# Kernel tuning notes

Hardware: AMD Instinct MI355X
Metric: run time of the kernel (lower is better)

## Reference

```python
import jax, jax.numpy as jnp
import numpy as np

BLOCK_SIZE = 32
FORMAT_MAX = 1.0
MANTISSA_BITS = 3.0   # E4M3-like element quantization
CYCLE_BUDGET = 16.0   # B_final: MSD cycle budget per output channel
ONLINE_DELAY = 2.0    # delta: online multiplier startup delay
NEG_LOG2 = -60.0


def _safe_log2(x):
    # log2 mapping 0 / negative to a large negative number
    return jnp.where(x > 0, jnp.log2(jnp.maximum(x, 1e-45)), NEG_LOG2)


def _quantize_elements(xn):
    # round-to-nearest float with MANTISSA_BITS mantissa bits (values in [-1, 1])
    a = jnp.abs(xn)
    e = jnp.floor(_safe_log2(a))
    step = jnp.exp2(e - MANTISSA_BITS)
    return jnp.where(a > 0, jnp.round(xn / step) * step, 0.0)


def _quantize_to_blocks(x_blocks, eps=1e-30):
    # x_blocks: (..., nb, bs) -> (x_q same shape, scales (..., nb))
    max_abs = jnp.max(jnp.abs(x_blocks), axis=-1)
    scales = jnp.maximum(max_abs / FORMAT_MAX, eps)
    x_q = _quantize_elements(x_blocks / scales[..., None])
    return x_q, scales


def _compute_inter_block_delays(w_scales, x_scales):
    # w_scales: (out, nb), x_scales: (N, nb)
    combined_log2 = _safe_log2(x_scales)[:, None, :] + _safe_log2(w_scales)[None, :, :]
    combined_e = jnp.floor(combined_log2)                 # (N, out, nb)
    e_max = jnp.max(combined_e, axis=-1)                  # (N, out)
    return e_max[..., None] - combined_e, e_max


def _compute_intra_block_delays(x_q_blocks):
    # x_q_blocks: (N, nb, bs)
    abs_vals = jnp.abs(x_q_blocks)
    elem_log2 = jnp.where(abs_vals > 0,
                          jnp.floor(jnp.log2(jnp.maximum(abs_vals, 1e-45))),
                          NEG_LOG2)
    e_max_block = jnp.max(elem_log2, axis=-1, keepdims=True)
    return e_max_block - elem_log2


def _msd_truncate(value, num_digits):
    # keep the `num_digits` most-significant NAF (non-adjacent form) digits
    abs_v = jnp.abs(value)
    sign = jnp.sign(value)
    mask = (num_digits > 0) & (abs_v > 0)
    msb_pos = jnp.floor(jnp.log2(jnp.maximum(abs_v, 1e-45)))
    scale_up = jnp.exp2(jnp.clip(23.0 - msb_pos, -126.0, 126.0))
    x_scaled = jnp.round(abs_v * scale_up).astype(jnp.int32)   # ~2^23..2^24
    x_h = x_scaled >> 1
    s = x_scaled + x_h
    naf_pos = s & ~x_h
    naf_neg = x_h & ~s
    combined = naf_pos | naf_neg
    naf_width = jnp.where(
        combined > 0,
        jnp.floor(jnp.log2(jnp.maximum(combined.astype(jnp.float32), 1.0))).astype(jnp.int32) + 1,
        jnp.zeros_like(combined))
    drop = jnp.clip(naf_width - num_digits.astype(jnp.int32), 0, 31)
    keep_mask = ~((jnp.int32(1) << drop) - 1)
    recon = ((naf_pos & keep_mask).astype(jnp.float32)
             - (naf_neg & keep_mask).astype(jnp.float32)) / scale_up
    return jnp.where(mask, sign * recon, 0.0)


def setup_inputs() -> dict:
    key = jax.random.key(0)
    k1, k2, k3 = jax.random.split(key, 3)
    N, in_f, out_f = 128, 1024, 512
    x = jax.random.normal(k1, (N, in_f), dtype=jnp.float32)
    weight = jax.random.normal(k2, (out_f, in_f), dtype=jnp.float32) * 0.02
    bias = jax.random.normal(k3, (out_f,), dtype=jnp.float32) * 0.01
    return {"x": x, "weight": weight, "bias": bias}


def reference(x, weight, bias):
    N, in_f = x.shape
    out_f = weight.shape[0]
    nb = in_f // BLOCK_SIZE
    xb = x.reshape(N, nb, BLOCK_SIZE)
    wb = weight.reshape(out_f, nb, BLOCK_SIZE)
    x_q, x_s = _quantize_to_blocks(xb)   # (N, nb, bs), (N, nb)
    w_q, w_s = _quantize_to_blocks(wb)   # (out, nb, bs), (out, nb)
    inter, e_max = _compute_inter_block_delays(w_s, x_s)  # (N, out, nb)
    intra = _compute_intra_block_delays(x_q)              # (N, nb, bs)
    # effective NAF digit budget per product element
    eff = (CYCLE_BUDGET - ONLINE_DELAY) - inter[..., None] - intra[:, None, :, :]
    prod = x_q[:, None, :, :] * w_q[None, :, :, :]        # (N, out, nb, bs)
    trunc = jax.lax.stop_gradient(_msd_truncate(prod, eff))  # torch.no_grad
    block_dots = jnp.sum(trunc, axis=-1)                  # (N, out, nb)
    out = jnp.einsum('nb,ob,nob->no', x_s, w_s, block_dots) + bias
    return out
```

## Files before the change

kernel.cpp:

```cpp
#include <hip/hip_runtime.h>
#include <cstdint>


#define NN 128
#define KF 1024
#define OF 512
#define NB 32
#define KS 32


__global__ __launch_bounds__(256) void prep_kernel(
    const float* __restrict__ x, const float* __restrict__ w,
    uint2* __restrict__ xaP2, uint2* __restrict__ wB,
    float* __restrict__ lxT, float* __restrict__ lw) {
  int bid = blockIdx.x;
  int tid = (int)threadIdx.x;
  bool is_x = bid < 512;
  int eid = is_x ? bid * 256 + tid : (bid - 512) * 256 + tid;
  float v = is_x ? x[eid] : w[eid];
  float a = fabsf(v);
  float m = a;
  #pragma unroll
  for (int s = 1; s < 32; s <<= 1) m = fmaxf(m, __shfl_xor(m, s, 32));
  float scale = fmaxf(m, 1e-30f);
  float xn = v / scale;
  unsigned nb_ = __float_as_uint(xn);
  unsigned ab = nb_ & 0x7fffffffu;
  bool zz = ab < 0x00800000u;
  int e = (int)(ab >> 23) - 127;
  float am = __uint_as_float((ab & 0x007fffffu) | 0x3f800000u);
  int mi = (int)rintf(am * 8.0f);
  if (mi == 16) { mi = 8; ++e; }
  if (zz) mi = 0;
  unsigned sgn = nb_ & 0x80000000u;
  unsigned sb = __float_as_uint(scale);
  if (is_x) {
    int di = zz ? 63 : min(-e, 63);
    unsigned fb = zz ? 0u : ((sb + (((unsigned)e) << 23)) | sgn);
    unsigned meta = (unsigned)mi | ((unsigned)di << 8);
    int k = eid & 1023, n = eid >> 10;
    xaP2[((k >> 1) * NN + n) * 2 + (k & 1)] = make_uint2(fb, meta);
    if ((tid & 31) == 0) lxT[(k >> 5) * NN + n] = log2f(scale);
  } else {
    unsigned fb = zz ? 0u : ((sb + (((unsigned)(e - 7)) << 23)) | sgn);
    wB[eid] = make_uint2(fb, (unsigned)mi);
    int o = eid >> 10, k = eid & 1023;
    if ((tid & 31) == 0) lw[o * NB + (k >> 5)] = log2f(scale);
  }
}

__global__ __launch_bounds__(256) void emax_kernel(
    const float* __restrict__ lxT, const float* __restrict__ lw,
    float* __restrict__ emaxT) {
  int gid = blockIdx.x * 256 + (int)threadIdx.x;
  int n = gid & (NN - 1), o = gid >> 7;
  float m = -1e30f;
  #pragma unroll
  for (int b = 0; b < NB; ++b)
    m = fmaxf(m, floorf(lxT[b * NN + n] + lw[o * NB + b]));
  emaxT[o * NN + n] = m;
}

__device__ __forceinline__ void prod_acc(int mx, int di, float fxs,
                                         unsigned fwbits, int mw, int nb,
                                         float& acc) {
  int p  = __mul24(mx, mw);
  int s3 = (p << 1) + p;
  int cx = s3 ^ p;
  int wd = 32 - __clz(cx);
  int u  = wd + di + nb;
  int drop = min(max(u, 0), wd);
  unsigned keep = 0xFFFFFFFFu << drop;
  unsigned kc = keep & (unsigned)cx;
  int r = (int)((unsigned)s3 & kc) - (int)((unsigned)p & kc);
  acc = fmaf((float)r * fxs, __uint_as_float(fwbits), acc);
}

__global__ __launch_bounds__(256, 4) void main_kernel(
    const uint4* __restrict__ xaP, const uint2* __restrict__ wB,
    const float* __restrict__ lxT, const float* __restrict__ lw,
    const float* __restrict__ emaxT, float* __restrict__ part) {
  __shared__ __align__(16) uint2 tile[32 * 32];
  int bid = blockIdx.x;
  int s   = bid & 31;
  int og  = (bid >> 5) & 15;
  int ng  = bid >> 9;
  int tid = (int)threadIdx.x, lane = tid & 63, w4 = tid >> 6;
  int o_base = og * 32;
  int k0 = s * 32;
  int n = ng * 64 + lane;

  {
    int r = tid >> 3, c = tid & 7;
    const uint4* src = reinterpret_cast<const uint4*>(&wB[(o_base + r) * KF + k0]);
    uint4* dst = reinterpret_cast<uint4*>(&tile[r * 32]);
    dst[c] = src[c];
    dst[c + 8] = src[c + 8];
  }

  int ow = o_base + w4 * 8;
  float lxv = lxT[s * NN + n];
  float acc[8];
  int nbv[8];
  #pragma unroll
  for (int j = 0; j < 8; ++j) {
    acc[j] = 0.f;
    float em = emaxT[(ow + j) * NN + n];
    nbv[j] = -(int)(14.0f - em + floorf(lxv + lw[(ow + j) * NB + s]));
  }
  __syncthreads();

  const uint4* xaRow = &xaP[(size_t)(k0 >> 1) * NN + n];
#define LDT(j, g) (*reinterpret_cast<const uint4*>(&tile[(w4 * 8 + (j)) * 32 + 2 * (g)]))
#define COMPUTE4(xv, t0, t1, t2, t3, J)                                    \
  {                                                                        \
    int mx0 = (int)(xv.y & 255u), di0 = (int)(xv.y >> 8);                  \
    int mx1 = (int)(xv.w & 255u), di1 = (int)(xv.w >> 8);                  \
    float fx0 = __uint_as_float(xv.x), fx1 = __uint_as_float(xv.z);        \
    prod_acc(mx0, di0, fx0, t0.x, (int)t0.y, nbv[J + 0], acc[J + 0]);      \
    prod_acc(mx1, di1, fx1, t0.z, (int)t0.w, nbv[J + 0], acc[J + 0]);      \
    prod_acc(mx0, di0, fx0, t1.x, (int)t1.y, nbv[J + 1], acc[J + 1]);      \
    prod_acc(mx1, di1, fx1, t1.z, (int)t1.w, nbv[J + 1], acc[J + 1]);      \
    prod_acc(mx0, di0, fx0, t2.x, (int)t2.y, nbv[J + 2], acc[J + 2]);      \
    prod_acc(mx1, di1, fx1, t2.z, (int)t2.w, nbv[J + 2], acc[J + 2]);      \
    prod_acc(mx0, di0, fx0, t3.x, (int)t3.y, nbv[J + 3], acc[J + 3]);      \
    prod_acc(mx1, di1, fx1, t3.z, (int)t3.w, nbv[J + 3], acc[J + 3]);      \
  }

  uint4 xa_ = xaRow[0];
  #pragma unroll 1
  for (int g = 0; g < 16; ++g) {
    uint4 xn_ = xaRow[(size_t)(g + 1) * NN];
    {
      uint4 t0 = LDT(0, g), t1 = LDT(1, g), t2 = LDT(2, g), t3 = LDT(3, g);
      COMPUTE4(xa_, t0, t1, t2, t3, 0);
    }
    {
      uint4 t0 = LDT(4, g), t1 = LDT(5, g), t2 = LDT(6, g), t3 = LDT(7, g);
      COMPUTE4(xa_, t0, t1, t2, t3, 4);
    }
    xa_ = xn_;
  }

  #pragma unroll
  for (int j = 0; j < 8; ++j)
    part[((size_t)(s * OF) + ow + j) * NN + n] = acc[j];
#undef COMPUTE4
#undef LDT
}

__global__ __launch_bounds__(256) void reduce_kernel(
    const float* __restrict__ part, const float* __restrict__ bias,
    float* __restrict__ out) {
  int gid = blockIdx.x * 256 + (int)threadIdx.x;
  int n = gid & (NN - 1), o = gid >> 7;
  float sum = bias[o];
  #pragma unroll
  for (int c = 0; c < KS; ++c) sum += part[((size_t)c * OF + o) * NN + n];
  out[n * OF + o] = sum;
}

extern "C" void kernel_launch(void* const* d_in, const int* in_sizes, int n_in,
                              void* d_out, int out_size, void* d_ws, size_t ws_size,
                              hipStream_t stream) {
  const float* x    = (const float*)d_in[0];
  const float* w    = (const float*)d_in[1];
  const float* bias = (const float*)d_in[2];
  float* out = (float*)d_out;
  char* ws = (char*)d_ws;
  uint2* xaP2  = (uint2*)(ws);
  uint4* xaP   = (uint4*)(ws);
  uint2* wB    = (uint2*)(ws + 1048576);
  float* lxT   = (float*)(ws + 5242880);
  float* lw    = (float*)(ws + 5259264);
  float* emaxT = (float*)(ws + 5324800);
  float* part  = (float*)(ws + 5580800);

  prep_kernel<<<2560, 256, 0, stream>>>(x, w, xaP2, wB, lxT, lw);
  emax_kernel<<<256, 256, 0, stream>>>(lxT, lw, emaxT);
  main_kernel<<<1024, 256, 0, stream>>>(xaP, wB, lxT, lw, emaxT, part);
  reduce_kernel<<<256, 256, 0, stream>>>(part, bias, out);
}
```

Baseline: 100.4 us.

## Replace per-product NAF truncation arithmetic with shared-memory lookup table

Builds an 11x16x16 table in LDS that holds the truncated NAF product value for each clamped digit budget and each pair of mantissa codes. The mantissa codes are pre-shifted in the prep kernel so the table offset is formed with adds. The inner loop then does one LDS gather per product instead of the multiply, clz, shift and mask chain. Each block now covers 16 output channels instead of 32, which doubles the grid and raises the occupancy hint to 8 blocks per CU. The cost is table construction in every block and possible LDS bank conflicts on the scattered lookups.

Measured after the change: 103.6 us. 1.03x slower.

```diff
diff --git a/kernel.cpp b/kernel.cpp
--- a/kernel.cpp
+++ b/kernel.cpp
@@ -37,13 +37,13 @@
   if (is_x) {
     int di = zz ? 63 : min(-e, 63);
     unsigned fb = zz ? 0u : ((sb + (((unsigned)e) << 23)) | sgn);
-    unsigned meta = (unsigned)mi | ((unsigned)di << 8);
+    unsigned meta = ((unsigned)mi << 6) | ((unsigned)di << 12);
     int k = eid & 1023, n = eid >> 10;
     xaP2[((k >> 1) * NN + n) * 2 + (k & 1)] = make_uint2(fb, meta);
     if ((tid & 31) == 0) lxT[(k >> 5) * NN + n] = log2f(scale);
   } else {
     unsigned fb = zz ? 0u : ((sb + (((unsigned)(e - 7)) << 23)) | sgn);
-    wB[eid] = make_uint2(fb, (unsigned)mi);
+    wB[eid] = make_uint2(fb, (unsigned)(mi << 2));
     int o = eid >> 10, k = eid & 1023;
     if ((tid & 31) == 0) lw[o * NB + (k >> 5)] = log2f(scale);
   }
@@ -61,91 +61,82 @@
   emaxT[o * NN + n] = m;
 }
 
-__device__ __forceinline__ void prod_acc(int mx, int di, float fxs,
-                                         unsigned fwbits, int mw, int nb,
-                                         float& acc) {
-  int p  = __mul24(mx, mw);
-  int s3 = (p << 1) + p;
-  int cx = s3 ^ p;
-  int wd = 32 - __clz(cx);
-  int u  = wd + di + nb;
-  int drop = min(max(u, 0), wd);
-  unsigned keep = 0xFFFFFFFFu << drop;
-  unsigned kc = keep & (unsigned)cx;
-  int r = (int)((unsigned)s3 & kc) - (int)((unsigned)p & kc);
-  acc = fmaf((float)r * fxs, __uint_as_float(fwbits), acc);
-}
-
-__global__ __launch_bounds__(256, 4) void main_kernel(
+__global__ __launch_bounds__(256, 8) void main_kernel(
     const uint4* __restrict__ xaP, const uint2* __restrict__ wB,
     const float* __restrict__ lxT, const float* __restrict__ lw,
     const float* __restrict__ emaxT, float* __restrict__ part) {
-  __shared__ __align__(16) uint2 tile[32 * 32];
+  __shared__ float lut[2816];
+  __shared__ __align__(16) uint2 tile[16 * 32];
   int bid = blockIdx.x;
   int s   = bid & 31;
-  int og  = (bid >> 5) & 15;
-  int ng  = bid >> 9;
+  int og  = (bid >> 5) & 31;
+  int ng  = bid >> 10;
   int tid = (int)threadIdx.x, lane = tid & 63, w4 = tid >> 6;
-  int o_base = og * 32;
+  int o_base = og * 16;
   int k0 = s * 32;
   int n = ng * 64 + lane;
 
+  #pragma unroll 1
+  for (int i = tid; i < 2816; i += 256) {
+    int effc = i >> 8, mx = (i >> 4) & 15, mw = i & 15;
+    int p  = mx * mw;
+    int s3 = 3 * p;
+    unsigned cx = (unsigned)(s3 ^ p);
+    int wd = 32 - __clz(cx);
+    int drop = max(wd - effc, 0);
+    unsigned kc = (0xFFFFFFFFu << drop) & cx;
+    int r = (int)((unsigned)s3 & kc) - (int)((unsigned)p & kc);
+    lut[i] = (float)r;
+  }
   {
-    int r = tid >> 3, c = tid & 7;
+    int r = tid >> 4, c = tid & 15;
     const uint4* src = reinterpret_cast<const uint4*>(&wB[(o_base + r) * KF + k0]);
-    uint4* dst = reinterpret_cast<uint4*>(&tile[r * 32]);
-    dst[c] = src[c];
-    dst[c + 8] = src[c + 8];
+    reinterpret_cast<uint4*>(&tile[r * 32])[c] = src[c];
   }
 
-  int ow = o_base + w4 * 8;
+  int ow = o_base + w4 * 4;
   float lxv = lxT[s * NN + n];
-  float acc[8];
-  int nbv[8];
+  float acc[4];
+  int bv[4];
   #pragma unroll
-  for (int j = 0; j < 8; ++j) {
+  for (int j = 0; j < 4; ++j) {
     acc[j] = 0.f;
     float em = emaxT[(ow + j) * NN + n];
-    nbv[j] = -(int)(14.0f - em + floorf(lxv + lw[(ow + j) * NB + s]));
+    bv[j] = (int)(14.0f - em + floorf(lxv + lw[(ow + j) * NB + s]));
   }
   __syncthreads();
 
   const uint4* xaRow = &xaP[(size_t)(k0 >> 1) * NN + n];
-#define LDT(j, g) (*reinterpret_cast<const uint4*>(&tile[(w4 * 8 + (j)) * 32 + 2 * (g)]))
-#define COMPUTE4(xv, t0, t1, t2, t3, J)                                    \
+  const char* lutB = (const char*)lut;
+#define LDT(j, g) (*reinterpret_cast<const uint4*>(&tile[(w4 * 4 + (j)) * 32 + 2 * (g)]))
+#define PROD(J, T, MX64, DI, FXS, HI)                                      \
   {                                                                        \
-    int mx0 = (int)(xv.y & 255u), di0 = (int)(xv.y >> 8);                  \
-    int mx1 = (int)(xv.w & 255u), di1 = (int)(xv.w >> 8);                  \
-    float fx0 = __uint_as_float(xv.x), fx1 = __uint_as_float(xv.z);        \
-    prod_acc(mx0, di0, fx0, t0.x, (int)t0.y, nbv[J + 0], acc[J + 0]);      \
-    prod_acc(mx1, di1, fx1, t0.z, (int)t0.w, nbv[J + 0], acc[J + 0]);      \
-    prod_acc(mx0, di0, fx0, t1.x, (int)t1.y, nbv[J + 1], acc[J + 1]);      \
-    prod_acc(mx1, di1, fx1, t1.z, (int)t1.w, nbv[J + 1], acc[J + 1]);      \
-    prod_acc(mx0, di0, fx0, t2.x, (int)t2.y, nbv[J + 2], acc[J + 2]);      \
-    prod_acc(mx1, di1, fx1, t2.z, (int)t2.w, nbv[J + 2], acc[J + 2]);      \
-    prod_acc(mx0, di0, fx0, t3.x, (int)t3.y, nbv[J + 3], acc[J + 3]);      \
-    prod_acc(mx1, di1, fx1, t3.z, (int)t3.w, nbv[J + 3], acc[J + 3]);      \
+    int e_ = min(max(bv[J] - (DI), 0), 10);                                \
+    int bx_ = (e_ << 10) + ((MX64) + (int)((HI) ? (T).w : (T).y));         \
+    float lv_ = *(const float*)(lutB + bx_);                               \
+    float f_ = (FXS) * __uint_as_float((HI) ? (T).z : (T).x);              \
+    acc[J] = fmaf(lv_, f_, acc[J]);                                        \
   }
 
   uint4 xa_ = xaRow[0];
-  #pragma unroll 1
+  #pragma unroll 2
   for (int g = 0; g < 16; ++g) {
     uint4 xn_ = xaRow[(size_t)(g + 1) * NN];
-    {
-      uint4 t0 = LDT(0, g), t1 = LDT(1, g), t2 = LDT(2, g), t3 = LDT(3, g);
-      COMPUTE4(xa_, t0, t1, t2, t3, 0);
-    }
-    {
-      uint4 t0 = LDT(4, g), t1 = LDT(5, g), t2 = LDT(6, g), t3 = LDT(7, g);
-      COMPUTE4(xa_, t0, t1, t2, t3, 4);
-    }
+    int mx64_0 = (int)(xa_.y & 0x3C0u), di0 = (int)(xa_.y >> 12);
+    int mx64_1 = (int)(xa_.w & 0x3C0u), di1 = (int)(xa_.w >> 12);
+    float fx0 = __uint_as_float(xa_.x), fx1 = __uint_as_float(xa_.z);
+    uint4 t0 = LDT(0, g), t1 = LDT(1, g), t2 = LDT(2, g), t3 = LDT(3, g);
+    PROD(0, t0, mx64_0, di0, fx0, 0); PROD(0, t0, mx64_1, di1, fx1, 1);
+    PROD(1, t1, mx64_0, di0, fx0, 0); PROD(1, t1, mx64_1, di1, fx1, 1);
+    PROD(2, t2, mx64_0, di0, fx0, 0); PROD(2, t2, mx64_1, di1, fx1, 1);
+    PROD(3, t3, mx64_0, di0, fx0, 0); PROD(3, t3, mx64_1, di1, fx1, 1);
     xa_ = xn_;
   }
 
   #pragma unroll
-  for (int j = 0; j < 8; ++j)
+  for (int j = 0; j < 4; ++j)
     part[((size_t)(s * OF) + ow + j) * NN + n] = acc[j];
-#undef COMPUTE4
+#undef PROD
 #undef LDT
 }
 
@@ -178,6 +169,6 @@
 
   prep_kernel<<<2560, 256, 0, stream>>>(x, w, xaP2, wB, lxT, lw);
   emax_kernel<<<256, 256, 0, stream>>>(lxT, lw, emaxT);
-  main_kernel<<<1024, 256, 0, stream>>>(xaP, wB, lxT, lw, emaxT, part);
+  main_kernel<<<2048, 256, 0, stream>>>(xaP, wB, lxT, lw, emaxT, part);
   reduce_kernel<<<256, 256, 0, stream>>>(part, bias, out);
 }
```
